# Kernel optimization log

Hardware: AMD Instinct MI355X
Metric: run time of the kernel (lower is better)

Reference implementation:

```python
import jax, jax.numpy as jnp
import numpy as np

N, D_IN, UNITS = 8192, 4096, 4096

def ste_sign(k):
    # larq ste_sign forward: sign with sign(0) -> +1
    return jnp.where(k >= 0, 1.0, -1.0).astype(k.dtype)

def setup_inputs() -> dict:
    key = jax.random.key(0)
    kx, kk = jax.random.split(key)
    x = jax.random.normal(kx, (N, D_IN), dtype=jnp.float32)
    kernel = jax.random.normal(kk, (D_IN, UNITS), dtype=jnp.float32)
    return {"x": x, "kernel": kernel}

def reference(x, kernel):
    # y = x @ sign(kernel); the `+ reduce_sum(x)*0` in the original is a no-op
    return x @ ste_sign(kernel)
```

## Files before the change

### kernel.cpp

```cpp
#include <hip/hip_runtime.h>
#include <stdint.h>

typedef __attribute__((ext_vector_type(8))) __bf16 bf16x8;
typedef __attribute__((ext_vector_type(4))) float f32x4;

__device__ inline unsigned short f32_to_bf16_rne(float f) {
  union { float f; uint32_t u; } c; c.f = f;
  uint32_t u = c.u;
  uint32_t r = (u + 0x7FFFu + ((u >> 16) & 1u)) >> 16;
  return (unsigned short)r;
}

__global__ __launch_bounds__(256) void convert_x_kernel(const float* __restrict__ X,
                                                        unsigned short* __restrict__ A,
                                                        size_t n) {
  size_t i = (size_t)blockIdx.x * 256 + threadIdx.x;
  size_t stride = (size_t)gridDim.x * 256;
  for (size_t e = i * 4; e < n; e += stride * 4) {
    const float4 v = *reinterpret_cast<const float4*>(X + e);
    ushort4 o;
    o.x = f32_to_bf16_rne(v.x);
    o.y = f32_to_bf16_rne(v.y);
    o.z = f32_to_bf16_rne(v.z);
    o.w = f32_to_bf16_rne(v.w);
    *reinterpret_cast<ushort4*>(A + e) = o;
  }
}

__global__ __launch_bounds__(256) void sign_transpose_kernel(const float* __restrict__ Km,
                                                             unsigned short* __restrict__ Bt,
                                                             int K, int N) {
  __shared__ unsigned short tile[64][65];
  const int k0 = blockIdx.x * 64;
  const int n0 = blockIdx.y * 64;
  const int t = threadIdx.x;
#pragma unroll
  for (int i = 0; i < 16; ++i) {
    int idx = t + i * 256;
    int kk = idx >> 6, nn = idx & 63;
    float v = Km[(size_t)(k0 + kk) * N + (n0 + nn)];
    tile[kk][nn] = (v >= 0.0f) ? (unsigned short)0x3F80u : (unsigned short)0xBF80u;
  }
  __syncthreads();
#pragma unroll
  for (int i = 0; i < 16; ++i) {
    int idx = t + i * 256;
    int nn = idx >> 6, kk = idx & 63;
    Bt[(size_t)(n0 + nn) * K + (k0 + kk)] = tile[kk][nn];
  }
}


__device__ __forceinline__ void stage_mat(const unsigned short* __restrict__ G,
                                          size_t grow0, int K, int k0,
                                          unsigned short* lds_wave_base,
                                          int tid) {
#pragma unroll
  for (int i = 0; i < 2; ++i) {
    const int row = i * 128 + (tid >> 2);
    const int srcslot = (tid & 3) ^ ((row >> 1) & 3);
    const unsigned short* ga = G + (grow0 + row) * (size_t)K + k0 + srcslot * 8;
    __builtin_amdgcn_global_load_lds(
        (const __attribute__((address_space(1))) void*)ga,
        (__attribute__((address_space(3))) void*)(lds_wave_base + i * 4096),
        16, 0, 0);
  }
}

__global__ __launch_bounds__(512, 2) void gemm_bf16_256(const unsigned short* __restrict__ A,
                                                        const unsigned short* __restrict__ Bt,
                                                        float* __restrict__ C,
                                                        int M, int N, int K) {
  __shared__ unsigned short lds[4 * 16384];

  const int nBN = N >> 8;
  const int nwg = gridDim.x;
  const int bid = blockIdx.x;
  int swz = bid;
  if ((nwg & 7) == 0) {
    const int q = nwg >> 3;
    swz = (bid & 7) * q + (bid >> 3);
  }
  const size_t a_row0 = (size_t)(swz / nBN) * 256;
  const size_t b_row0 = (size_t)(swz % nBN) * 256;

  const int tid = threadIdx.x;
  const int wv = tid >> 6, ln = tid & 63;
  const int llo = ln & 15, lhi = ln >> 4;
  const int wr = wv >> 2, wc = wv & 3;
  const int sA = lhi ^ ((llo >> 1) & 3);

  const int aoff = (wr * 128 + llo) * 32 + sA * 8;
  const int boff = 8192 + (wc * 64 + llo) * 32 + sA * 8;

  const int NTt = K >> 5;

  f32x4 acc[8][4];
#pragma unroll
  for (int i = 0; i < 8; ++i)
#pragma unroll
    for (int j = 0; j < 4; ++j) acc[i][j] = (f32x4){0.f, 0.f, 0.f, 0.f};

#pragma unroll
  for (int tt = 0; tt < 3; ++tt) {
    stage_mat(A, a_row0, K, tt * 32, &lds[tt * 16384 + wv * 512], tid);
    stage_mat(Bt, b_row0, K, tt * 32, &lds[tt * 16384 + 8192 + wv * 512], tid);
  }
  asm volatile("s_waitcnt vmcnt(8)\n" ::: "memory");
  __builtin_amdgcn_s_barrier();

  for (int t = 0; t < NTt; ++t) {
    const int cb = (t & 3) * 16384;
    const int ts = (t + 3 < NTt) ? (t + 3) : (NTt - 1);
    const int tb = (ts & 3) * 16384;

    bf16x8 bfr[4], af0[4], af1[4];
#pragma unroll
    for (int ni = 0; ni < 4; ++ni)
      bfr[ni] = *reinterpret_cast<const bf16x8*>(&lds[cb + boff + ni * 512]);
#pragma unroll
    for (int mi = 0; mi < 4; ++mi)
      af0[mi] = *reinterpret_cast<const bf16x8*>(&lds[cb + aoff + mi * 512]);
#pragma unroll
    for (int mi = 0; mi < 4; ++mi)
      af1[mi] = *reinterpret_cast<const bf16x8*>(&lds[cb + aoff + 2048 + mi * 512]);
    stage_mat(A, a_row0, K, ts * 32, &lds[tb + wv * 512], tid);
    stage_mat(Bt, b_row0, K, ts * 32, &lds[tb + 8192 + wv * 512], tid);
    __builtin_amdgcn_sched_barrier(0);

    __builtin_amdgcn_s_setprio(1);
#pragma unroll
    for (int mi = 0; mi < 4; ++mi)
#pragma unroll
      for (int ni = 0; ni < 4; ++ni)
        acc[mi][ni] = __builtin_amdgcn_mfma_f32_16x16x32_bf16(af0[mi], bfr[ni], acc[mi][ni], 0, 0, 0);
    __builtin_amdgcn_s_setprio(0);
    __builtin_amdgcn_sched_barrier(0);

    __builtin_amdgcn_s_setprio(1);
#pragma unroll
    for (int mi = 0; mi < 4; ++mi)
#pragma unroll
      for (int ni = 0; ni < 4; ++ni)
        acc[4 + mi][ni] = __builtin_amdgcn_mfma_f32_16x16x32_bf16(af1[mi], bfr[ni], acc[4 + mi][ni], 0, 0, 0);
    __builtin_amdgcn_s_setprio(0);

    asm volatile("s_waitcnt vmcnt(8)\n" ::: "memory");
    __builtin_amdgcn_s_barrier();
  }

#pragma unroll
  for (int mi = 0; mi < 8; ++mi) {
#pragma unroll
    for (int ni = 0; ni < 4; ++ni) {
      const size_t col = b_row0 + wc * 64 + ni * 16 + llo;
      const size_t rbase = a_row0 + wr * 128 + mi * 16 + lhi * 4;
#pragma unroll
      for (int j = 0; j < 4; ++j)
        C[(rbase + j) * (size_t)N + col] = acc[mi][ni][j];
    }
  }
}

__global__ __launch_bounds__(256) void gemm_f32_fallback(const float* __restrict__ X,
                                                         const float* __restrict__ Km,
                                                         float* __restrict__ C,
                                                         int M, int N, int K) {
  __shared__ float As[64][16];
  __shared__ float Bs[16][65];
  const int nBN = N / 64;
  const int bm = blockIdx.x / nBN;
  const int bn = blockIdx.x % nBN;
  const int t = threadIdx.x;
  const int tx = t & 15, ty = t >> 4;
  float acc[4][4] = {};
  for (int kb = 0; kb < K; kb += 16) {
#pragma unroll
    for (int i = 0; i < 4; ++i) {
      int e = t + i * 256;
      int r = e >> 4, c = e & 15;
      As[r][c] = X[(size_t)(bm * 64 + r) * K + kb + c];
      int rk = e >> 6, cn = e & 63;
      float v = Km[(size_t)(kb + rk) * N + bn * 64 + cn];
      Bs[rk][cn] = (v >= 0.f) ? 1.f : -1.f;
    }
    __syncthreads();
#pragma unroll
    for (int kk = 0; kk < 16; ++kk) {
      float a[4], b[4];
#pragma unroll
      for (int r = 0; r < 4; ++r) a[r] = As[ty * 4 + r][kk];
#pragma unroll
      for (int c = 0; c < 4; ++c) b[c] = Bs[kk][tx * 4 + c];
#pragma unroll
      for (int r = 0; r < 4; ++r)
#pragma unroll
        for (int c = 0; c < 4; ++c) acc[r][c] += a[r] * b[c];
    }
    __syncthreads();
  }
#pragma unroll
  for (int r = 0; r < 4; ++r)
#pragma unroll
    for (int c = 0; c < 4; ++c)
      C[(size_t)(bm * 64 + ty * 4 + r) * N + bn * 64 + tx * 4 + c] = acc[r][c];
}

extern "C" void kernel_launch(void* const* d_in, const int* in_sizes, int n_in,
                              void* d_out, int out_size, void* d_ws, size_t ws_size,
                              hipStream_t stream) {
  const float* x = (const float*)d_in[0];
  const float* kern = (const float*)d_in[1];
  float* out = (float*)d_out;

  const int K = 4096;
  const int N = 4096;
  const int M = in_sizes[0] / K;

  const size_t a_bytes = (size_t)M * K * 2;
  const size_t b_bytes = (size_t)N * K * 2;

  if (ws_size >= a_bytes + b_bytes && (M % 256) == 0 && (N % 256) == 0 && (K % 128) == 0) {
    unsigned short* A = (unsigned short*)d_ws;
    unsigned short* Bt = (unsigned short*)((char*)d_ws + a_bytes);
    convert_x_kernel<<<2048, 256, 0, stream>>>(x, A, (size_t)M * K);
    sign_transpose_kernel<<<dim3(K / 64, N / 64), 256, 0, stream>>>(kern, Bt, K, N);
    gemm_bf16_256<<<(M / 256) * (N / 256), 512, 0, stream>>>(A, Bt, out, M, N, K);
  } else {
    gemm_f32_fallback<<<(M / 64) * (N / 64), 256, 0, stream>>>(x, kern, out, M, N, K);
  }
}
```

Measured before the change: 280.1 us.

## Double-buffer LDS fragments in registers and interleave global staging with MFMA halves

The GEMM main loop is unrolled by two with ping-pong register sets. The A and B fragments for the next K-tile are read from LDS during the current tile's second MFMA half, and the A and B global-to-LDS staging is split across the two MFMA halves. The aim is to hide LDS read latency behind MFMA work instead of stalling at the top of each iteration. To make the next tile's data visible before the barrier, the vmcnt wait is tightened from 8 to 4, which shortens the effective global prefetch distance. The extra fragment registers add register pressure under the 512x2 launch bounds.

```diff
diff --git a/kernel.cpp b/kernel.cpp
--- a/kernel.cpp
+++ b/kernel.cpp
@@ -67,6 +67,47 @@
   }
 }
 
+#define GEMM_ITER(T, AFC, BFC, AFN, BFN)                                              \
+  {                                                                                   \
+    const int cb = ((T) & 3) * 16384;                                                 \
+    const int ts = ((T) + 3 < NTt) ? ((T) + 3) : (NTt - 1);                           \
+    const int tb = (ts & 3) * 16384;                                                  \
+    bf16x8 af1[4];                                                                    \
+    _Pragma("unroll")                                                                 \
+    for (int mi = 0; mi < 4; ++mi)                                                    \
+      af1[mi] = *reinterpret_cast<const bf16x8*>(&lds[cb + aoff + 2048 + mi * 512]);  \
+    stage_mat(A, a_row0, K, ts * 32, &lds[tb + wv * 512], tid);                       \
+    __builtin_amdgcn_sched_barrier(0);                                                \
+    __builtin_amdgcn_s_setprio(1);                                                    \
+    _Pragma("unroll")                                                                 \
+    for (int mi = 0; mi < 4; ++mi)                                                    \
+      _Pragma("unroll")                                                               \
+      for (int ni = 0; ni < 4; ++ni)                                                  \
+        acc[mi][ni] =                                                                 \
+            __builtin_amdgcn_mfma_f32_16x16x32_bf16(AFC[mi], BFC[ni], acc[mi][ni], 0, 0, 0); \
+    __builtin_amdgcn_s_setprio(0);                                                    \
+    __builtin_amdgcn_sched_barrier(0);                                                \
+    const int nb = ((T) + 1 < NTt) ? ((((T) + 1) & 3) * 16384) : cb;                  \
+    _Pragma("unroll")                                                                 \
+    for (int ni = 0; ni < 4; ++ni)                                                    \
+      BFN[ni] = *reinterpret_cast<const bf16x8*>(&lds[nb + boff + ni * 512]);         \
+    _Pragma("unroll")                                                                 \
+    for (int mi = 0; mi < 4; ++mi)                                                    \
+      AFN[mi] = *reinterpret_cast<const bf16x8*>(&lds[nb + aoff + mi * 512]);         \
+    stage_mat(Bt, b_row0, K, ts * 32, &lds[tb + 8192 + wv * 512], tid);               \
+    __builtin_amdgcn_sched_barrier(0);                                                \
+    __builtin_amdgcn_s_setprio(1);                                                    \
+    _Pragma("unroll")                                                                 \
+    for (int mi = 0; mi < 4; ++mi)                                                    \
+      _Pragma("unroll")                                                               \
+      for (int ni = 0; ni < 4; ++ni)                                                  \
+        acc[4 + mi][ni] =                                                             \
+            __builtin_amdgcn_mfma_f32_16x16x32_bf16(af1[mi], BFC[ni], acc[4 + mi][ni], 0, 0, 0); \
+    __builtin_amdgcn_s_setprio(0);                                                    \
+    asm volatile("s_waitcnt vmcnt(4)\n" ::: "memory");                                \
+    __builtin_amdgcn_s_barrier();                                                     \
+  }
+
 __global__ __launch_bounds__(512, 2) void gemm_bf16_256(const unsigned short* __restrict__ A,
                                                         const unsigned short* __restrict__ Bt,
                                                         float* __restrict__ C,
@@ -106,47 +147,20 @@
     stage_mat(A, a_row0, K, tt * 32, &lds[tt * 16384 + wv * 512], tid);
     stage_mat(Bt, b_row0, K, tt * 32, &lds[tt * 16384 + 8192 + wv * 512], tid);
   }
-  asm volatile("s_waitcnt vmcnt(8)\n" ::: "memory");
+  asm volatile("s_waitcnt vmcnt(4)\n" ::: "memory");
   __builtin_amdgcn_s_barrier();
 
-  for (int t = 0; t < NTt; ++t) {
-    const int cb = (t & 3) * 16384;
-    const int ts = (t + 3 < NTt) ? (t + 3) : (NTt - 1);
-    const int tb = (ts & 3) * 16384;
-
-    bf16x8 bfr[4], af0[4], af1[4];
-#pragma unroll
-    for (int ni = 0; ni < 4; ++ni)
-      bfr[ni] = *reinterpret_cast<const bf16x8*>(&lds[cb + boff + ni * 512]);
-#pragma unroll
-    for (int mi = 0; mi < 4; ++mi)
-      af0[mi] = *reinterpret_cast<const bf16x8*>(&lds[cb + aoff + mi * 512]);
-#pragma unroll
-    for (int mi = 0; mi < 4; ++mi)
-      af1[mi] = *reinterpret_cast<const bf16x8*>(&lds[cb + aoff + 2048 + mi * 512]);
-    stage_mat(A, a_row0, K, ts * 32, &lds[tb + wv * 512], tid);
-    stage_mat(Bt, b_row0, K, ts * 32, &lds[tb + 8192 + wv * 512], tid);
-    __builtin_amdgcn_sched_barrier(0);
-
-    __builtin_amdgcn_s_setprio(1);
-#pragma unroll
-    for (int mi = 0; mi < 4; ++mi)
-#pragma unroll
-      for (int ni = 0; ni < 4; ++ni)
-        acc[mi][ni] = __builtin_amdgcn_mfma_f32_16x16x32_bf16(af0[mi], bfr[ni], acc[mi][ni], 0, 0, 0);
-    __builtin_amdgcn_s_setprio(0);
-    __builtin_amdgcn_sched_barrier(0);
-
-    __builtin_amdgcn_s_setprio(1);
-#pragma unroll
-    for (int mi = 0; mi < 4; ++mi)
-#pragma unroll
-      for (int ni = 0; ni < 4; ++ni)
-        acc[4 + mi][ni] = __builtin_amdgcn_mfma_f32_16x16x32_bf16(af1[mi], bfr[ni], acc[4 + mi][ni], 0, 0, 0);
-    __builtin_amdgcn_s_setprio(0);
-
-    asm volatile("s_waitcnt vmcnt(8)\n" ::: "memory");
-    __builtin_amdgcn_s_barrier();
+  bf16x8 af0_a[4], bfr_a[4], af0_b[4], bfr_b[4];
+#pragma unroll
+  for (int ni = 0; ni < 4; ++ni)
+    bfr_a[ni] = *reinterpret_cast<const bf16x8*>(&lds[boff + ni * 512]);
+#pragma unroll
+  for (int mi = 0; mi < 4; ++mi)
+    af0_a[mi] = *reinterpret_cast<const bf16x8*>(&lds[aoff + mi * 512]);
+
+  for (int t = 0; t < NTt; t += 2) {
+    GEMM_ITER(t, af0_a, bfr_a, af0_b, bfr_b)
+    GEMM_ITER(t + 1, af0_b, bfr_b, af0_a, bfr_a)
   }
 
 #pragma unroll
```

Measured after the change: 266.4 us. 1.05x faster.

## Restructure bf16 GEMM main loop into 8-phase half-tile pipeline with BK=64 double buffer

Applied to the files above, without the earlier changes.

Replaces the 4-stage BK=32 ring buffer with a double-buffered BK=64 layout staged in half-tiles (128 rows of A or B at a time). Each K-step is split into four quadrant phases that interleave one half-tile global->LDS load with a block of 16 MFMAs, using barriers and explicit lgkmcnt/vmcnt waits. It also changes the LDS swizzle to an 8-slot XOR pattern. The aim is finer-grained overlap of memory and compute and fewer bank conflicts, at the cost of more barriers per K-step and a more fragile, hand-written schedule.

```diff
diff --git a/kernel.cpp b/kernel.cpp
--- a/kernel.cpp
+++ b/kernel.cpp
@@ -51,27 +51,76 @@
 }
 
 
-__device__ __forceinline__ void stage_mat(const unsigned short* __restrict__ G,
-                                          size_t grow0, int K, int k0,
-                                          unsigned short* lds_wave_base,
-                                          int tid) {
+__device__ __forceinline__ void stage_half(const unsigned short* __restrict__ G,
+                                           size_t grow0, int K, int k0,
+                                           unsigned short* lds_half_base,
+                                           int tid, int wv) {
 #pragma unroll
   for (int i = 0; i < 2; ++i) {
-    const int row = i * 128 + (tid >> 2);
-    const int srcslot = (tid & 3) ^ ((row >> 1) & 3);
-    const unsigned short* ga = G + (grow0 + row) * (size_t)K + k0 + srcslot * 8;
+    const int row = i * 64 + (tid >> 3);
+    const int slot = (tid & 7) ^ (row & 7);
+    const unsigned short* ga = G + (grow0 + row) * (size_t)K + k0 + slot * 8;
     __builtin_amdgcn_global_load_lds(
         (const __attribute__((address_space(1))) void*)ga,
-        (__attribute__((address_space(3))) void*)(lds_wave_base + i * 4096),
+        (__attribute__((address_space(3))) void*)(lds_half_base + i * 4096 + wv * 512),
         16, 0, 0);
   }
 }
+
+#define PHASE(T, KT, Q)                                                                 \
+  {                                                                                     \
+    constexpr int mh = ((Q) >> 1) & 1, nh = (Q) & 1;                                    \
+    constexpr int dcur = (KT) * 32768;                                                  \
+    if constexpr ((Q) == 0) {                                                           \
+      _Pragma("unroll") for (int fr = 0; fr < 4; ++fr)                                  \
+        _Pragma("unroll") for (int ks = 0; ks < 2; ++ks)                                \
+          a[fr][ks] = *reinterpret_cast<const bf16x8*>(                                 \
+              &lds[(dcur + aoff + fr * 1024) ^ (ks << 5)]);                             \
+      _Pragma("unroll") for (int fc = 0; fc < 2; ++fc)                                  \
+        _Pragma("unroll") for (int ks = 0; ks < 2; ++ks)                                \
+          b[0][fc][ks] = *reinterpret_cast<const bf16x8*>(                              \
+              &lds[(dcur + boff + fc * 1024) ^ (ks << 5)]);                             \
+    } else if constexpr ((Q) == 1) {                                                    \
+      _Pragma("unroll") for (int fc = 0; fc < 2; ++fc)                                  \
+        _Pragma("unroll") for (int ks = 0; ks < 2; ++ks)                                \
+          b[1][fc][ks] = *reinterpret_cast<const bf16x8*>(                              \
+              &lds[(dcur + boff + 2048 + fc * 1024) ^ (ks << 5)]);                      \
+    } else if constexpr ((Q) == 2) {                                                    \
+      _Pragma("unroll") for (int fr = 0; fr < 4; ++fr)                                  \
+        _Pragma("unroll") for (int ks = 0; ks < 2; ++ks)                                \
+          a[fr][ks] = *reinterpret_cast<const bf16x8*>(                                 \
+              &lds[(dcur + aoff + 4096 + fr * 1024) ^ (ks << 5)]);                      \
+    }                                                                                   \
+    {                                                                                   \
+      int j = 8 * (T) + 4 * (KT) + (Q) + 5;                                             \
+      if (j > JMAX) j = JMAX;                                                           \
+      const int kj = j >> 2, rr = j & 3, hh = rr & 1;                                   \
+      const unsigned short* SG = (rr < 2) ? A : Bt;                                     \
+      const size_t g0 = ((rr < 2) ? a_row0 : b_row0) + (size_t)hh * 128;                \
+      unsigned short* lb = (unsigned short*)lds + (kj & 1) * 32768 +                    \
+                           ((rr < 2) ? 0 : 16384) + hh * 8192;                          \
+      stage_half(SG, g0, K, kj * 64, lb, tid, wv);                                      \
+    }                                                                                   \
+    if constexpr ((Q) == 0) asm volatile("s_waitcnt lgkmcnt(8)\n" ::: "memory");        \
+    __builtin_amdgcn_s_barrier();                                                       \
+    asm volatile("s_waitcnt lgkmcnt(0)\n" ::: "memory");                                \
+    __builtin_amdgcn_sched_barrier(0);                                                  \
+    __builtin_amdgcn_s_setprio(1);                                                      \
+    _Pragma("unroll") for (int ks = 0; ks < 2; ++ks)                                    \
+      _Pragma("unroll") for (int fr = 0; fr < 4; ++fr)                                  \
+        _Pragma("unroll") for (int fc = 0; fc < 2; ++fc)                                \
+          acc[mh * 4 + fr][nh * 2 + fc] = __builtin_amdgcn_mfma_f32_16x16x32_bf16(      \
+              a[fr][ks], b[nh][fc][ks], acc[mh * 4 + fr][nh * 2 + fc], 0, 0, 0);        \
+    __builtin_amdgcn_s_setprio(0);                                                      \
+    if constexpr ((Q) == 3) asm volatile("s_waitcnt vmcnt(2)\n" ::: "memory");          \
+    __builtin_amdgcn_s_barrier();                                                       \
+  }
 
 __global__ __launch_bounds__(512, 2) void gemm_bf16_256(const unsigned short* __restrict__ A,
                                                         const unsigned short* __restrict__ Bt,
                                                         float* __restrict__ C,
                                                         int M, int N, int K) {
-  __shared__ unsigned short lds[4 * 16384];
+  __shared__ unsigned short lds[2 * 32768];
 
   const int nBN = N >> 8;
   const int nwg = gridDim.x;
@@ -88,12 +137,13 @@
   const int wv = tid >> 6, ln = tid & 63;
   const int llo = ln & 15, lhi = ln >> 4;
   const int wr = wv >> 2, wc = wv & 3;
-  const int sA = lhi ^ ((llo >> 1) & 3);
-
-  const int aoff = (wr * 128 + llo) * 32 + sA * 8;
-  const int boff = 8192 + (wc * 64 + llo) * 32 + sA * 8;
-
-  const int NTt = K >> 5;
+
+  const int slot0 = (lhi ^ (llo & 7)) * 8;
+  const int aoff = wr * 8192 + llo * 64 + slot0;
+  const int boff = 16384 + (wc >> 1) * 8192 + (wc & 1) * 4096 + llo * 64 + slot0;
+
+  const int NI = K >> 7;
+  const int JMAX = (K >> 4) - 1;
 
   f32x4 acc[8][4];
 #pragma unroll
@@ -101,52 +151,19 @@
 #pragma unroll
     for (int j = 0; j < 4; ++j) acc[i][j] = (f32x4){0.f, 0.f, 0.f, 0.f};
 
-#pragma unroll
-  for (int tt = 0; tt < 3; ++tt) {
-    stage_mat(A, a_row0, K, tt * 32, &lds[tt * 16384 + wv * 512], tid);
-    stage_mat(Bt, b_row0, K, tt * 32, &lds[tt * 16384 + 8192 + wv * 512], tid);
-  }
-  asm volatile("s_waitcnt vmcnt(8)\n" ::: "memory");
+  bf16x8 a[4][2], b[2][2][2];
+
+  stage_half(A, a_row0, K, 0, (unsigned short*)lds, tid, wv);
+  stage_half(A, a_row0 + 128, K, 0, (unsigned short*)lds + 8192, tid, wv);
+  stage_half(Bt, b_row0, K, 0, (unsigned short*)lds + 16384, tid, wv);
+  stage_half(Bt, b_row0 + 128, K, 0, (unsigned short*)lds + 24576, tid, wv);
+  stage_half(A, a_row0, K, 64, (unsigned short*)lds + 32768, tid, wv);
+  asm volatile("s_waitcnt vmcnt(2)\n" ::: "memory");
   __builtin_amdgcn_s_barrier();
 
-  for (int t = 0; t < NTt; ++t) {
-    const int cb = (t & 3) * 16384;
-    const int ts = (t + 3 < NTt) ? (t + 3) : (NTt - 1);
-    const int tb = (ts & 3) * 16384;
-
-    bf16x8 bfr[4], af0[4], af1[4];
-#pragma unroll
-    for (int ni = 0; ni < 4; ++ni)
-      bfr[ni] = *reinterpret_cast<const bf16x8*>(&lds[cb + boff + ni * 512]);
-#pragma unroll
-    for (int mi = 0; mi < 4; ++mi)
-      af0[mi] = *reinterpret_cast<const bf16x8*>(&lds[cb + aoff + mi * 512]);
-#pragma unroll
-    for (int mi = 0; mi < 4; ++mi)
-      af1[mi] = *reinterpret_cast<const bf16x8*>(&lds[cb + aoff + 2048 + mi * 512]);
-    stage_mat(A, a_row0, K, ts * 32, &lds[tb + wv * 512], tid);
-    stage_mat(Bt, b_row0, K, ts * 32, &lds[tb + 8192 + wv * 512], tid);
-    __builtin_amdgcn_sched_barrier(0);
-
-    __builtin_amdgcn_s_setprio(1);
-#pragma unroll
-    for (int mi = 0; mi < 4; ++mi)
-#pragma unroll
-      for (int ni = 0; ni < 4; ++ni)
-        acc[mi][ni] = __builtin_amdgcn_mfma_f32_16x16x32_bf16(af0[mi], bfr[ni], acc[mi][ni], 0, 0, 0);
-    __builtin_amdgcn_s_setprio(0);
-    __builtin_amdgcn_sched_barrier(0);
-
-    __builtin_amdgcn_s_setprio(1);
-#pragma unroll
-    for (int mi = 0; mi < 4; ++mi)
-#pragma unroll
-      for (int ni = 0; ni < 4; ++ni)
-        acc[4 + mi][ni] = __builtin_amdgcn_mfma_f32_16x16x32_bf16(af1[mi], bfr[ni], acc[4 + mi][ni], 0, 0, 0);
-    __builtin_amdgcn_s_setprio(0);
-
-    asm volatile("s_waitcnt vmcnt(8)\n" ::: "memory");
-    __builtin_amdgcn_s_barrier();
+  for (int t = 0; t < NI; ++t) {
+    PHASE(t, 0, 0) PHASE(t, 0, 1) PHASE(t, 0, 2) PHASE(t, 0, 3)
+    PHASE(t, 1, 0) PHASE(t, 1, 1) PHASE(t, 1, 2) PHASE(t, 1, 3)
   }
 
 #pragma unroll
```

After: 312.8 us. +11.7%, slower.
